# Kernel tuning notes

Hardware: AMD Instinct MI355X
Metric: run time of the kernel (lower is better)

Reference implementation:

```python
import math
import jax, jax.numpy as jnp
import numpy as np

B, N, DIM, H, DH = 2, 1024, 1024, 16, 64
SCALE = 16.0  # cosine_sim_scale
LN_EPS = 1e-5


def layer_norm(x, g, eps=LN_EPS):
    # torch: unbiased=False variance
    m = jnp.mean(x, axis=-1, keepdims=True)
    v = jnp.var(x, axis=-1, keepdims=True)
    return (x - m) * jax.lax.rsqrt(v + eps) * g


def l2norm(t):
    # F.normalize(dim=-1): x / max(||x||, 1e-12)
    n = jnp.linalg.norm(t, axis=-1, keepdims=True)
    return t / jnp.maximum(n, 1e-12)


def setup_inputs() -> dict:
    key = jax.random.key(0)
    ks = jax.random.split(key, 8)
    x = jax.random.normal(ks[0], (B, N, DIM), jnp.float32)
    attn_bias = jax.random.normal(ks[1], (B, H, N, N + 1), jnp.float32) * 0.02
    g_in = jnp.ones((DIM,), jnp.float32)
    w_q = jax.random.normal(ks[2], (H * DH, DIM), jnp.float32) * 0.02
    w_kv = jax.random.normal(ks[3], (2 * DH, DIM), jnp.float32) * 0.02
    null_kv = jax.random.normal(ks[4], (2, DH), jnp.float32)
    w_out = jax.random.normal(ks[5], (DIM, H * DH), jnp.float32) * 0.02
    g_out = jnp.ones((DIM,), jnp.float32)
    mask = jnp.ones((B, N), dtype=bool)
    return dict(x=x, attn_bias=attn_bias, g_in=g_in, w_q=w_q, w_kv=w_kv,
                null_kv=null_kv, w_out=w_out, g_out=g_out, mask=mask)


def reference(x, attn_bias, g_in, w_q, w_kv, null_kv, w_out, g_out, mask):
    b, n, _ = x.shape
    xn = layer_norm(x, g_in)
    q = xn @ w_q.T                      # [b, n, H*DH]
    kv = xn @ w_kv.T                    # [b, n, 2*DH]  (single kv head)
    k, v = kv[..., :DH], kv[..., DH:]
    q = q.reshape(b, n, H, DH).transpose(0, 2, 1, 3) * SCALE  # [b, h, n, d]
    nk = jnp.broadcast_to(null_kv[0], (b, 1, DH))
    nv = jnp.broadcast_to(null_kv[1], (b, 1, DH))
    k = jnp.concatenate([nk, k], axis=1)  # [b, n+1, d]
    v = jnp.concatenate([nv, v], axis=1)
    # cosine-sim attention: l2norm then scale by sqrt(cosine_sim_scale)
    q = l2norm(q) * math.sqrt(SCALE)
    k = l2norm(k) * math.sqrt(SCALE)
    sim = jnp.einsum('bhid,bjd->bhij', q, k) + attn_bias
    mask_p = jnp.concatenate([jnp.ones((b, 1), dtype=bool), mask], axis=1)  # null kv always visible
    max_neg = -jnp.finfo(sim.dtype).max
    sim = jnp.where(mask_p[:, None, None, :], sim, max_neg)
    attn = jax.nn.softmax(sim.astype(jnp.float32), axis=-1).astype(sim.dtype)
    out = jnp.einsum('bhij,bjd->bhid', attn, v)
    out = out.transpose(0, 2, 1, 3).reshape(b, n, H * DH)
    out = out @ w_out.T
    return layer_norm(out, g_out)
```

## Files before the change

kernel.cpp:

```cpp
#include <hip/hip_runtime.h>
#include <math.h>

#define B_   2
#define N_   1024
#define DIM_ 1024
#define H_   16
#define NK_  1025
#define NKP_ 1088

typedef __attribute__((ext_vector_type(8))) short s16x8;
typedef __attribute__((ext_vector_type(4))) float f32x4;

__device__ __forceinline__ float wave_sum(float v) {
  #pragma unroll
  for (int off = 32; off; off >>= 1) v += __shfl_xor(v, off);
  return v;
}
__device__ __forceinline__ short f2bf(float f) {
  union { float f; unsigned u; } v; v.f = f;
  unsigned r = (v.u + 0x7fffu + ((v.u >> 16) & 1u)) >> 16;
  return (short)r;
}
__device__ __forceinline__ float bf2f(short s) {
  union { unsigned u; float f; } v; v.u = ((unsigned)(unsigned short)s) << 16;
  return v.f;
}
__device__ __forceinline__ void gl_lds16(const short* g, short* lds) {
  __builtin_amdgcn_global_load_lds(
      (const __attribute__((address_space(1))) void*)g,
      (__attribute__((address_space(3))) void*)lds, 16, 0, 0);
}

__global__ __launch_bounds__(256) void cvt_all(const float* __restrict__ wq,
                                               const float* __restrict__ wkv,
                                               const float* __restrict__ wout,
                                               short* __restrict__ Wqkv,
                                               short* __restrict__ Wout) {
  int i = (blockIdx.x * 256 + threadIdx.x) * 4;
  const float* s; short* d; int k;
  if (i < 1048576)      { s = wq;   d = Wqkv;           k = i; }
  else if (i < 1179648) { s = wkv;  d = Wqkv + 1048576; k = i - 1048576; }
  else                  { s = wout; d = Wout;           k = i - 1179648; }
  float4 v = *(const float4*)&s[k];
  short4 r; r.x = f2bf(v.x); r.y = f2bf(v.y); r.z = f2bf(v.z); r.w = f2bf(v.w);
  *(short4*)&d[k] = r;
}

__global__ __launch_bounds__(256) void ln_in(const float* __restrict__ x,
                                             const float* __restrict__ g,
                                             short* __restrict__ o) {
  int row = blockIdx.x, tid = threadIdx.x;
  const float* xr = x + (size_t)row * DIM_;
  float4 v = *(const float4*)&xr[tid * 4];
  float s  = v.x + v.y + v.z + v.w;
  float sq = v.x*v.x + v.y*v.y + v.z*v.z + v.w*v.w;
  s = wave_sum(s); sq = wave_sum(sq);
  __shared__ float red[8];
  int w = tid >> 6, lane = tid & 63;
  if (lane == 0) { red[w] = s; red[4 + w] = sq; }
  __syncthreads();
  s  = red[0] + red[1] + red[2] + red[3];
  sq = red[4] + red[5] + red[6] + red[7];
  float mean = s * (1.0f / DIM_);
  float var  = sq * (1.0f / DIM_) - mean * mean;
  float inv  = rsqrtf(var + 1e-5f);
  float4 g4 = *(const float4*)&g[tid * 4];
  short4 r;
  r.x = f2bf((v.x - mean) * inv * g4.x);
  r.y = f2bf((v.y - mean) * inv * g4.y);
  r.z = f2bf((v.z - mean) * inv * g4.z);
  r.w = f2bf((v.w - mean) * inv * g4.w);
  *(short4*)&o[(size_t)row * DIM_ + tid * 4] = r;
}

__global__ __launch_bounds__(256) void ln_out(const short* __restrict__ xb,
                                              const float* __restrict__ g,
                                              float* __restrict__ o) {
  int row = blockIdx.x, tid = threadIdx.x;
  const short* xr = xb + (size_t)row * DIM_;
  short4 s4 = *(const short4*)&xr[tid * 4];
  float v0 = bf2f(s4.x), v1 = bf2f(s4.y), v2 = bf2f(s4.z), v3 = bf2f(s4.w);
  float s  = v0 + v1 + v2 + v3;
  float sq = v0*v0 + v1*v1 + v2*v2 + v3*v3;
  s = wave_sum(s); sq = wave_sum(sq);
  __shared__ float red[8];
  int w = tid >> 6, lane = tid & 63;
  if (lane == 0) { red[w] = s; red[4 + w] = sq; }
  __syncthreads();
  s  = red[0] + red[1] + red[2] + red[3];
  sq = red[4] + red[5] + red[6] + red[7];
  float mean = s * (1.0f / DIM_);
  float var  = sq * (1.0f / DIM_) - mean * mean;
  float inv  = rsqrtf(var + 1e-5f);
  float4 g4 = *(const float4*)&g[tid * 4];
  float4 r;
  r.x = (v0 - mean) * inv * g4.x;
  r.y = (v1 - mean) * inv * g4.y;
  r.z = (v2 - mean) * inv * g4.z;
  r.w = (v3 - mean) * inv * g4.w;
  *(float4*)&o[(size_t)row * DIM_ + tid * 4] = r;
}

__global__ __launch_bounds__(256) void gemm_bf(const short* __restrict__ A,
                                               const short* __restrict__ W,
                                               short* __restrict__ C,
                                               int M, int Nn, int K) {
  __shared__ short sb[2][24 * 512];
  int tid = threadIdx.x, l = tid & 63, w = tid >> 6;
  int li = l & 15, lg = l >> 4;
  int m0 = blockIdx.y * 64, n0 = blockIdx.x * 128;
  int wm = w & 1, wn = w >> 1;

  const short* src[6];
  #pragma unroll
  for (int s = 0; s < 6; ++s) {
    int c6 = w * 6 + s;
    if (c6 < 8) { int cm = c6 >> 1, ck = c6 & 1;
      src[s] = A + (size_t)(m0 + cm * 16 + li) * K + ck * 32 + lg * 8;
    } else { int cw = c6 - 8, cn = cw >> 1, ck = cw & 1;
      src[s] = W + (size_t)(n0 + cn * 16 + li) * K + ck * 32 + lg * 8;
    }
  }

  f32x4 acc[2][4];
  #pragma unroll
  for (int mi = 0; mi < 2; ++mi)
    #pragma unroll
    for (int ni = 0; ni < 4; ++ni) {
      acc[mi][ni][0] = 0.f; acc[mi][ni][1] = 0.f;
      acc[mi][ni][2] = 0.f; acc[mi][ni][3] = 0.f;
    }

  #pragma unroll
  for (int s = 0; s < 6; ++s) gl_lds16(src[s], &sb[0][(w * 6 + s) * 512]);
  __syncthreads();

  int KT = K >> 6, cur = 0;
  for (int kt = 0; kt < KT; ++kt) {
    if (kt + 1 < KT) {
      #pragma unroll
      for (int s = 0; s < 6; ++s)
        gl_lds16(src[s] + (size_t)(kt + 1) * 64, &sb[cur ^ 1][(w * 6 + s) * 512]);
    }
    const short* sc = &sb[cur][0];
    #pragma unroll
    for (int ck = 0; ck < 2; ++ck) {
      s16x8 a0 = *(const s16x8*)&sc[((wm * 2 + 0) * 2 + ck) * 512 + l * 8];
      s16x8 a1 = *(const s16x8*)&sc[((wm * 2 + 1) * 2 + ck) * 512 + l * 8];
      #pragma unroll
      for (int ni = 0; ni < 4; ++ni) {
        s16x8 bf = *(const s16x8*)&sc[(8 + (wn * 4 + ni) * 2 + ck) * 512 + l * 8];
        acc[0][ni] = __builtin_amdgcn_mfma_f32_16x16x32_bf16(a0, bf, acc[0][ni], 0, 0, 0);
        acc[1][ni] = __builtin_amdgcn_mfma_f32_16x16x32_bf16(a1, bf, acc[1][ni], 0, 0, 0);
      }
    }
    __syncthreads();
    cur ^= 1;
  }
  #pragma unroll
  for (int mi = 0; mi < 2; ++mi)
    #pragma unroll
    for (int ni = 0; ni < 4; ++ni)
      #pragma unroll
      for (int rr = 0; rr < 4; ++rr)
        C[(size_t)(m0 + wm * 32 + mi * 16 + lg * 4 + rr) * Nn
          + n0 + wn * 64 + ni * 16 + li] = f2bf(acc[mi][ni][rr]);
}

__global__ __launch_bounds__(256) void prep_all(const short* __restrict__ Cq,
                                                const float* __restrict__ nullkv,
                                                short* __restrict__ Qbh,
                                                short* __restrict__ Kf,
                                                short* __restrict__ Vf) {
  int bidx = blockIdx.x;
  int l = threadIdx.x & 63, w = threadIdx.x >> 6;
  if (bidx < 8192) {
    int gid = bidx * 4 + w;
    int m = gid >> 4, h = gid & 15;
    float v = bf2f(Cq[(size_t)m * 1152 + h * 64 + l]);
    float ss = wave_sum(v * v);
    float q = v * (4.0f / fmaxf(sqrtf(ss), 1e-12f));
    int b = m >> 10, i = m & 1023;
    Qbh[(((size_t)(b * H_ + h)) * N_ + i) * 64 + l] = f2bf(q);
  } else {
    int row = (bidx - 8192) * 4 + w;
    int b = row / NKP_, j = row % NKP_;
    float kk, vv;
    if (j == 0)       { kk = nullkv[l]; vv = nullkv[64 + l]; }
    else if (j < NK_) {
      size_t m = (size_t)b * 1024 + j - 1;
      kk = bf2f(Cq[m * 1152 + 1024 + l]);
      vv = bf2f(Cq[m * 1152 + 1088 + l]);
    } else            { kk = 0.f; vv = 0.f; }
    float n = sqrtf(wave_sum(kk * kk));
    kk = kk * (4.0f / fmaxf(n, 1e-12f));
    Kf[(((size_t)b * 68 + (j >> 4)) * 2 + (l >> 5)) * 512
       + (size_t)((((l >> 3) & 3) << 4) + (j & 15)) * 8 + (l & 7)] = f2bf(kk);
    Vf[(((size_t)b * 17 + (j >> 6)) * 8 + ((l >> 4) << 1) + ((j >> 5) & 1)) * 512
       + (size_t)((((j >> 3) & 3) << 4) + (l & 15)) * 8 + (j & 7)] = f2bf(vv);
  }
}

__global__ __launch_bounds__(256, 2) void attn_v5(const short* __restrict__ Qbh,
                                                  const short* __restrict__ Kf,
                                                  const short* __restrict__ Vf,
                                                  const float* __restrict__ bias,
                                                  short* __restrict__ O) {
  __shared__ short sb[2][16 * 512];
  __shared__ short sP[4][1024];

  int tid = threadIdx.x, l = tid & 63, w = tid >> 6;
  int li = l & 15, lg = l >> 4;
  int bid = blockIdx.x;
  int it = bid & 15, h = (bid >> 4) & 15, b = bid >> 8;
  int i0 = it * 64 + w * 16;

  const short* qbase = Qbh + (((size_t)(b * H_ + h)) * N_ + i0 + li) * 64 + lg * 8;
  s16x8 qf0 = *(const s16x8*)qbase;
  s16x8 qf1 = *(const s16x8*)(qbase + 32);

  const short* kfb = Kf + (size_t)b * 68 * 2 * 512;
  const short* vfb = Vf + (size_t)b * 17 * 8 * 512;
  const float* bptr = bias + ((size_t)(b * H_ + h) * N_ + i0 + li) * NK_;

  #pragma unroll
  for (int s = 0; s < 2; ++s) {
    gl_lds16(kfb + (2 * w + s) * 512 + l * 8, &sb[0][(2 * w + s) * 512]);
    gl_lds16(vfb + (2 * w + s) * 512 + l * 8, &sb[0][(8 + 2 * w + s) * 512]);
  }

  s16x8 kl0 = *(const s16x8*)&kfb[((size_t)64 * 2 + 0) * 512 + lg * 128];
  s16x8 kl1 = *(const s16x8*)&kfb[((size_t)64 * 2 + 1) * 512 + lg * 128];
  float se = 0.f;
  #pragma unroll
  for (int e = 0; e < 8; ++e)
    se += bf2f(qf0[e]) * bf2f(kl0[e]) + bf2f(qf1[e]) * bf2f(kl1[e]);
  se += __shfl_xor(se, 16);
  se += __shfl_xor(se, 32);
  se += bptr[1024];

  float m_ = se, l_ = 1.f;
  f32x4 o[4];
  #pragma unroll
  for (int dt = 0; dt < 4; ++dt)
    #pragma unroll
    for (int rr = 0; rr < 4; ++rr)
      o[dt][rr] = bf2f(vfb[((size_t)16 * 8 + dt * 2) * 512 + (lg * 4 + rr) * 8]);

  float4 bb[3][4];
  #pragma unroll
  for (int q4 = 0; q4 < 4; ++q4) {
    bb[0][q4] = *(const float4*)(bptr + q4 * 16 + lg * 4);
    bb[1][q4] = *(const float4*)(bptr + 64 + q4 * 16 + lg * 4);
  }
  __syncthreads();

  short* pw = &sP[w][0];

  #pragma unroll
  for (int jt = 0; jt < 16; ++jt) {
    const int cb = jt & 1;
    if (jt + 1 < 16) {
      const short* kt_ = kfb + (size_t)(jt + 1) * 8 * 512;
      const short* vt_ = vfb + (size_t)(jt + 1) * 8 * 512;
      #pragma unroll
      for (int s = 0; s < 2; ++s) {
        gl_lds16(kt_ + (2 * w + s) * 512 + l * 8, &sb[cb ^ 1][(2 * w + s) * 512]);
        gl_lds16(vt_ + (2 * w + s) * 512 + l * 8, &sb[cb ^ 1][(8 + 2 * w + s) * 512]);
      }
    }
    if (jt + 2 < 16) {
      const float* bp = bptr + (jt + 2) * 64 + lg * 4;
      #pragma unroll
      for (int q4 = 0; q4 < 4; ++q4)
        bb[(jt + 2) % 3][q4] = *(const float4*)(bp + q4 * 16);
    }

    const short* sk = &sb[cb][0];
    const short* sv = &sb[cb][8 * 512];

    f32x4 st[4];
    #pragma unroll
    for (int jt4 = 0; jt4 < 4; ++jt4) {
      s16x8 ka0 = *(const s16x8*)&sk[(jt4 * 2 + 0) * 512 + l * 8];
      s16x8 ka1 = *(const s16x8*)&sk[(jt4 * 2 + 1) * 512 + l * 8];
      f32x4 cc; cc[0] = 0.f; cc[1] = 0.f; cc[2] = 0.f; cc[3] = 0.f;
      cc = __builtin_amdgcn_mfma_f32_16x16x32_bf16(ka0, qf0, cc, 0, 0, 0);
      cc = __builtin_amdgcn_mfma_f32_16x16x32_bf16(ka1, qf1, cc, 0, 0, 0);
      st[jt4] = cc;
    }

    float vmax = -1e30f;
    #pragma unroll
    for (int jt4 = 0; jt4 < 4; ++jt4)
      #pragma unroll
      for (int rr = 0; rr < 4; ++rr) {
        st[jt4][rr] += ((const float*)&bb[jt % 3][jt4])[rr];
        vmax = fmaxf(vmax, st[jt4][rr]);
      }
    vmax = fmaxf(vmax, __shfl_xor(vmax, 16));
    vmax = fmaxf(vmax, __shfl_xor(vmax, 32));
    float mnew = fmaxf(m_, vmax);
    float cre = __expf(m_ - mnew);
    m_ = mnew;
    float psum = 0.f;
    #pragma unroll
    for (int jt4 = 0; jt4 < 4; ++jt4)
      #pragma unroll
      for (int rr = 0; rr < 4; ++rr) {
        float p = __expf(st[jt4][rr] - mnew);
        st[jt4][rr] = p;
        psum += p;
      }
    psum += __shfl_xor(psum, 16);
    psum += __shfl_xor(psum, 32);
    l_ = l_ * cre + psum;
    #pragma unroll
    for (int dt = 0; dt < 4; ++dt) {
      o[dt][0] *= cre; o[dt][1] *= cre; o[dt][2] *= cre; o[dt][3] *= cre;
    }

    #pragma unroll
    for (int jt4 = 0; jt4 < 4; ++jt4) {
      int kfw = jt4 >> 1;
      int gw  = 2 * (jt4 & 1) + (lg >> 1);
      int ew  = (lg & 1) * 4;
      int off = kfw * 512 + (gw * 16 + li) * 8 + ew;
      #pragma unroll
      for (int rr = 0; rr < 4; ++rr) pw[off + rr] = f2bf(st[jt4][rr]);
    }
    s16x8 pb0 = *(const s16x8*)&pw[l * 8];
    s16x8 pb1 = *(const s16x8*)&pw[512 + l * 8];

    #pragma unroll
    for (int dt = 0; dt < 4; ++dt) {
      s16x8 va0 = *(const s16x8*)&sv[(dt * 2 + 0) * 512 + l * 8];
      s16x8 va1 = *(const s16x8*)&sv[(dt * 2 + 1) * 512 + l * 8];
      o[dt] = __builtin_amdgcn_mfma_f32_16x16x32_bf16(va0, pb0, o[dt], 0, 0, 0);
      o[dt] = __builtin_amdgcn_mfma_f32_16x16x32_bf16(va1, pb1, o[dt], 0, 0, 0);
    }
    __syncthreads();
  }

  float inv = 1.f / l_;
  size_t obase = ((size_t)(b * N_ + i0 + li) * H_ + h) * 64;
  #pragma unroll
  for (int dt = 0; dt < 4; ++dt)
    #pragma unroll
    for (int rp = 0; rp < 2; ++rp) {
      unsigned lo = (unsigned short)f2bf(o[dt][rp * 2]     * inv);
      unsigned hi = (unsigned short)f2bf(o[dt][rp * 2 + 1] * inv);
      *(unsigned*)&O[obase + dt * 16 + lg * 4 + rp * 2] = lo | (hi << 16);
    }
}

extern "C" void kernel_launch(void* const* d_in, const int* in_sizes, int n_in,
                              void* d_out, int out_size, void* d_ws, size_t ws_size,
                              hipStream_t stream) {
  (void)in_sizes; (void)n_in; (void)out_size; (void)ws_size;
  const float* x       = (const float*)d_in[0];
  const float* bias    = (const float*)d_in[1];
  const float* g_in    = (const float*)d_in[2];
  const float* w_q     = (const float*)d_in[3];
  const float* w_kv    = (const float*)d_in[4];
  const float* null_kv = (const float*)d_in[5];
  const float* w_out   = (const float*)d_in[6];
  const float* g_out   = (const float*)d_in[7];

  char* p = (char*)d_ws;
  short* XNbf = (short*)p;
  short* Wqkv = (short*)(p + 4194304);
  short* Wout = (short*)(p + 6553600);
  short* Cbf  = (short*)(p + 8650752);
  short* Qbh  = (short*)(p + 13369344);
  short* Kf   = (short*)(p + 17563648);
  short* Vf   = (short*)(p + 17842176);
  short* AOUT = XNbf;
  short* Cout = Cbf;
  float* out  = (float*)d_out;

  cvt_all<<<2176, 256, 0, stream>>>(w_q, w_kv, w_out, Wqkv, Wout);
  ln_in<<<B_ * N_, 256, 0, stream>>>(x, g_in, XNbf);
  gemm_bf<<<dim3(9, 32), 256, 0, stream>>>(XNbf, Wqkv, Cbf, B_ * N_, 1152, DIM_);
  prep_all<<<8192 + 544, 256, 0, stream>>>(Cbf, null_kv, Qbh, Kf, Vf);
  attn_v5<<<B_ * H_ * (N_ / 64), 256, 0, stream>>>(Qbh, Kf, Vf, bias, AOUT);
  gemm_bf<<<dim3(8, 32), 256, 0, stream>>>(AOUT, Wout, Cout, B_ * N_, DIM_, DIM_);
  ln_out<<<B_ * N_, 256, 0, stream>>>(Cout, g_out, out);
}
```

Baseline: 109.3 us.

## Split attention over key halves with a merge kernel; fuse weight cast and input layernorm

The attention kernel now splits the key range into two halves per query tile. This doubles the block count from 512 to 1024 and raises launch_bounds occupancy to 4. Partial outputs are stored as bf16 along with their running max and sum, and a new merge kernel combines them. Separately, the weight conversion and input layernorm kernels are fused into one launch to save a kernel launch. The split adds an extra kernel, extra global traffic, and a bf16 rounding step on the unnormalized partials.

```diff
diff --git a/kernel.cpp b/kernel.cpp
--- a/kernel.cpp
+++ b/kernel.cpp
@@ -31,25 +31,26 @@
       (__attribute__((address_space(3))) void*)lds, 16, 0, 0);
 }
 
-__global__ __launch_bounds__(256) void cvt_all(const float* __restrict__ wq,
-                                               const float* __restrict__ wkv,
-                                               const float* __restrict__ wout,
-                                               short* __restrict__ Wqkv,
-                                               short* __restrict__ Wout) {
-  int i = (blockIdx.x * 256 + threadIdx.x) * 4;
-  const float* s; short* d; int k;
-  if (i < 1048576)      { s = wq;   d = Wqkv;           k = i; }
-  else if (i < 1179648) { s = wkv;  d = Wqkv + 1048576; k = i - 1048576; }
-  else                  { s = wout; d = Wout;           k = i - 1179648; }
-  float4 v = *(const float4*)&s[k];
-  short4 r; r.x = f2bf(v.x); r.y = f2bf(v.y); r.z = f2bf(v.z); r.w = f2bf(v.w);
-  *(short4*)&d[k] = r;
-}
-
-__global__ __launch_bounds__(256) void ln_in(const float* __restrict__ x,
+__global__ __launch_bounds__(256) void pre_k(const float* __restrict__ wq,
+                                             const float* __restrict__ wkv,
+                                             const float* __restrict__ wout,
+                                             short* __restrict__ Wqkv,
+                                             short* __restrict__ Wout,
+                                             const float* __restrict__ x,
                                              const float* __restrict__ g,
-                                             short* __restrict__ o) {
-  int row = blockIdx.x, tid = threadIdx.x;
+                                             short* __restrict__ xo) {
+  if (blockIdx.x < 2176) {
+    int i = (blockIdx.x * 256 + threadIdx.x) * 4;
+    const float* s; short* d; int k;
+    if (i < 1048576)      { s = wq;   d = Wqkv;           k = i; }
+    else if (i < 1179648) { s = wkv;  d = Wqkv + 1048576; k = i - 1048576; }
+    else                  { s = wout; d = Wout;           k = i - 1179648; }
+    float4 v = *(const float4*)&s[k];
+    short4 r; r.x = f2bf(v.x); r.y = f2bf(v.y); r.z = f2bf(v.z); r.w = f2bf(v.w);
+    *(short4*)&d[k] = r;
+    return;
+  }
+  int row = blockIdx.x - 2176, tid = threadIdx.x;
   const float* xr = x + (size_t)row * DIM_;
   float4 v = *(const float4*)&xr[tid * 4];
   float s  = v.x + v.y + v.z + v.w;
@@ -70,7 +71,7 @@
   r.y = f2bf((v.y - mean) * inv * g4.y);
   r.z = f2bf((v.z - mean) * inv * g4.z);
   r.w = f2bf((v.w - mean) * inv * g4.w);
-  *(short4*)&o[(size_t)row * DIM_ + tid * 4] = r;
+  *(short4*)&xo[(size_t)row * DIM_ + tid * 4] = r;
 }
 
 __global__ __launch_bounds__(256) void ln_out(const short* __restrict__ xb,
@@ -201,19 +202,22 @@
   }
 }
 
-__global__ __launch_bounds__(256, 2) void attn_v5(const short* __restrict__ Qbh,
+__global__ __launch_bounds__(256, 4) void attn_v6(const short* __restrict__ Qbh,
                                                   const short* __restrict__ Kf,
                                                   const short* __restrict__ Vf,
                                                   const float* __restrict__ bias,
-                                                  short* __restrict__ O) {
+                                                  short* __restrict__ Opart,
+                                                  float* __restrict__ Mp,
+                                                  float* __restrict__ Lp) {
   __shared__ short sb[2][16 * 512];
   __shared__ short sP[4][1024];
 
   int tid = threadIdx.x, l = tid & 63, w = tid >> 6;
   int li = l & 15, lg = l >> 4;
   int bid = blockIdx.x;
-  int it = bid & 15, h = (bid >> 4) & 15, b = bid >> 8;
+  int half = bid & 1, it = (bid >> 1) & 15, h = (bid >> 5) & 15, b = bid >> 9;
   int i0 = it * 64 + w * 16;
+  const int t0 = half * 8;
 
   const short* qbase = Qbh + (((size_t)(b * H_ + h)) * N_ + i0 + li) * 64 + lg * 8;
   s16x8 qf0 = *(const s16x8*)qbase;
@@ -223,44 +227,55 @@
   const short* vfb = Vf + (size_t)b * 17 * 8 * 512;
   const float* bptr = bias + ((size_t)(b * H_ + h) * N_ + i0 + li) * NK_;
 
-  #pragma unroll
-  for (int s = 0; s < 2; ++s) {
-    gl_lds16(kfb + (2 * w + s) * 512 + l * 8, &sb[0][(2 * w + s) * 512]);
-    gl_lds16(vfb + (2 * w + s) * 512 + l * 8, &sb[0][(8 + 2 * w + s) * 512]);
-  }
-
-  s16x8 kl0 = *(const s16x8*)&kfb[((size_t)64 * 2 + 0) * 512 + lg * 128];
-  s16x8 kl1 = *(const s16x8*)&kfb[((size_t)64 * 2 + 1) * 512 + lg * 128];
-  float se = 0.f;
-  #pragma unroll
-  for (int e = 0; e < 8; ++e)
-    se += bf2f(qf0[e]) * bf2f(kl0[e]) + bf2f(qf1[e]) * bf2f(kl1[e]);
-  se += __shfl_xor(se, 16);
-  se += __shfl_xor(se, 32);
-  se += bptr[1024];
-
-  float m_ = se, l_ = 1.f;
+  {
+    const short* kt_ = kfb + (size_t)t0 * 8 * 512;
+    const short* vt_ = vfb + (size_t)t0 * 8 * 512;
+    #pragma unroll
+    for (int s = 0; s < 2; ++s) {
+      gl_lds16(kt_ + (2 * w + s) * 512 + l * 8, &sb[0][(2 * w + s) * 512]);
+      gl_lds16(vt_ + (2 * w + s) * 512 + l * 8, &sb[0][(8 + 2 * w + s) * 512]);
+    }
+  }
+
+  float m_, l_;
   f32x4 o[4];
-  #pragma unroll
-  for (int dt = 0; dt < 4; ++dt)
-    #pragma unroll
-    for (int rr = 0; rr < 4; ++rr)
-      o[dt][rr] = bf2f(vfb[((size_t)16 * 8 + dt * 2) * 512 + (lg * 4 + rr) * 8]);
-
-  float4 bb[3][4];
-  #pragma unroll
-  for (int q4 = 0; q4 < 4; ++q4) {
-    bb[0][q4] = *(const float4*)(bptr + q4 * 16 + lg * 4);
-    bb[1][q4] = *(const float4*)(bptr + 64 + q4 * 16 + lg * 4);
-  }
+  if (half == 0) {
+    s16x8 kl0 = *(const s16x8*)&kfb[((size_t)64 * 2 + 0) * 512 + lg * 128];
+    s16x8 kl1 = *(const s16x8*)&kfb[((size_t)64 * 2 + 1) * 512 + lg * 128];
+    float se = 0.f;
+    #pragma unroll
+    for (int e = 0; e < 8; ++e)
+      se += bf2f(qf0[e]) * bf2f(kl0[e]) + bf2f(qf1[e]) * bf2f(kl1[e]);
+    se += __shfl_xor(se, 16);
+    se += __shfl_xor(se, 32);
+    se += bptr[1024];
+    m_ = se; l_ = 1.f;
+    #pragma unroll
+    for (int dt = 0; dt < 4; ++dt)
+      #pragma unroll
+      for (int rr = 0; rr < 4; ++rr)
+        o[dt][rr] = bf2f(vfb[((size_t)16 * 8 + dt * 2) * 512 + (lg * 4 + rr) * 8]);
+  } else {
+    m_ = -1e30f; l_ = 0.f;
+    #pragma unroll
+    for (int dt = 0; dt < 4; ++dt) {
+      o[dt][0] = 0.f; o[dt][1] = 0.f; o[dt][2] = 0.f; o[dt][3] = 0.f;
+    }
+  }
+
+  float4 bb[2][4];
+  #pragma unroll
+  for (int q4 = 0; q4 < 4; ++q4)
+    bb[0][q4] = *(const float4*)(bptr + t0 * 64 + q4 * 16 + lg * 4);
   __syncthreads();
 
   short* pw = &sP[w][0];
 
   #pragma unroll
-  for (int jt = 0; jt < 16; ++jt) {
-    const int cb = jt & 1;
-    if (jt + 1 < 16) {
+  for (int t = 0; t < 8; ++t) {
+    const int cb = t & 1;
+    const int jt = t0 + t;
+    if (t + 1 < 8) {
       const short* kt_ = kfb + (size_t)(jt + 1) * 8 * 512;
       const short* vt_ = vfb + (size_t)(jt + 1) * 8 * 512;
       #pragma unroll
@@ -268,12 +283,10 @@
         gl_lds16(kt_ + (2 * w + s) * 512 + l * 8, &sb[cb ^ 1][(2 * w + s) * 512]);
         gl_lds16(vt_ + (2 * w + s) * 512 + l * 8, &sb[cb ^ 1][(8 + 2 * w + s) * 512]);
       }
-    }
-    if (jt + 2 < 16) {
-      const float* bp = bptr + (jt + 2) * 64 + lg * 4;
+      const float* bp = bptr + (jt + 1) * 64 + lg * 4;
       #pragma unroll
       for (int q4 = 0; q4 < 4; ++q4)
-        bb[(jt + 2) % 3][q4] = *(const float4*)(bp + q4 * 16);
+        bb[(t + 1) & 1][q4] = *(const float4*)(bp + q4 * 16);
     }
 
     const short* sk = &sb[cb][0];
@@ -295,7 +308,7 @@
     for (int jt4 = 0; jt4 < 4; ++jt4)
       #pragma unroll
       for (int rr = 0; rr < 4; ++rr) {
-        st[jt4][rr] += ((const float*)&bb[jt % 3][jt4])[rr];
+        st[jt4][rr] += ((const float*)&bb[t & 1][jt4])[rr];
         vmax = fmaxf(vmax, st[jt4][rr]);
       }
     vmax = fmaxf(vmax, __shfl_xor(vmax, 16));
@@ -342,14 +355,53 @@
     __syncthreads();
   }
 
-  float inv = 1.f / l_;
+  size_t slot = (size_t)bid * 256 + tid;
+  Mp[slot] = m_;
+  Lp[slot] = l_;
+  short* op = Opart + slot * 16;
+  #pragma unroll
+  for (int dt = 0; dt < 4; ++dt)
+    #pragma unroll
+    for (int rp = 0; rp < 2; ++rp) {
+      unsigned lo = (unsigned short)f2bf(o[dt][rp * 2]);
+      unsigned hi = (unsigned short)f2bf(o[dt][rp * 2 + 1]);
+      *(unsigned*)&op[dt * 4 + rp * 2] = lo | (hi << 16);
+    }
+}
+
+__global__ __launch_bounds__(256) void merge_k(const short* __restrict__ Opart,
+                                               const float* __restrict__ Mp,
+                                               const float* __restrict__ Lp,
+                                               short* __restrict__ O) {
+  int grp = blockIdx.x;
+  int s = threadIdx.x;
+  int it = grp & 15, h = (grp >> 4) & 15, b = grp >> 8;
+  size_t s0 = ((size_t)grp * 2 + 0) * 256 + s;
+  size_t s1 = ((size_t)grp * 2 + 1) * 256 + s;
+  float m0 = Mp[s0], m1 = Mp[s1];
+  float l0 = Lp[s0], l1 = Lp[s1];
+  float ms = fmaxf(m0, m1);
+  float f0 = __expf(m0 - ms), f1 = __expf(m1 - ms);
+  float inv = 1.0f / (l0 * f0 + l1 * f1);
+  f0 *= inv; f1 *= inv;
+  s16x8 o0a = *(const s16x8*)&Opart[s0 * 16];
+  s16x8 o0b = *(const s16x8*)&Opart[s0 * 16 + 8];
+  s16x8 o1a = *(const s16x8*)&Opart[s1 * 16];
+  s16x8 o1b = *(const s16x8*)&Opart[s1 * 16 + 8];
+  int w = s >> 6, l = s & 63, li = l & 15, lg = l >> 4;
+  int i0 = it * 64 + w * 16;
   size_t obase = ((size_t)(b * N_ + i0 + li) * H_ + h) * 64;
   #pragma unroll
   for (int dt = 0; dt < 4; ++dt)
     #pragma unroll
     for (int rp = 0; rp < 2; ++rp) {
-      unsigned lo = (unsigned short)f2bf(o[dt][rp * 2]     * inv);
-      unsigned hi = (unsigned short)f2bf(o[dt][rp * 2 + 1] * inv);
+      int k = dt * 4 + rp * 2;
+      float v0 = (k < 8 ? bf2f(o0a[k & 7]) : bf2f(o0b[k & 7])) * f0
+               + (k < 8 ? bf2f(o1a[k & 7]) : bf2f(o1b[k & 7])) * f1;
+      float v1 = (k + 1 < 8 ? bf2f(o0a[(k + 1) & 7]) : bf2f(o0b[(k + 1) & 7])) * f0
+               + (k + 1 < 8 ? bf2f(o1a[(k + 1) & 7]) : bf2f(o1b[(k + 1) & 7])) * f1;
+      unsigned lo = (unsigned short)f2bf(v0);
+      unsigned hi = (unsigned short)f2bf(v1);
       *(unsigned*)&O[obase + dt * 16 + lg * 4 + rp * 2] = lo | (hi << 16);
     }
 }
@@ -375,15 +427,18 @@
   short* Qbh  = (short*)(p + 13369344);
   short* Kf   = (short*)(p + 17563648);
   short* Vf   = (short*)(p + 17842176);
+  short* Opart= (short*)(p + 18120704);
+  float* Mp   = (float*)(p + 26509312);
+  float* Lp   = (float*)(p + 27557888);
   short* AOUT = XNbf;
   short* Cout = Cbf;
   float* out  = (float*)d_out;
 
-  cvt_all<<<2176, 256, 0, stream>>>(w_q, w_kv, w_out, Wqkv, Wout);
-  ln_in<<<B_ * N_, 256, 0, stream>>>(x, g_in, XNbf);
+  pre_k<<<2176 + 2048, 256, 0, stream>>>(w_q, w_kv, w_out, Wqkv, Wout, x, g_in, XNbf);
   gemm_bf<<<dim3(9, 32), 256, 0, stream>>>(XNbf, Wqkv, Cbf, B_ * N_, 1152, DIM_);
   prep_all<<<8192 + 544, 256, 0, stream>>>(Cbf, null_kv, Qbh, Kf, Vf);
-  attn_v5<<<B_ * H_ * (N_ / 64), 256, 0, stream>>>(Qbh, Kf, Vf, bias, AOUT);
+  attn_v6<<<B_ * H_ * (N_ / 64) * 2, 256, 0, stream>>>(Qbh, Kf, Vf, bias, Opart, Mp, Lp);
+  merge_k<<<B_ * H_ * (N_ / 64), 256, 0, stream>>>(Opart, Mp, Lp, AOUT);
   gemm_bf<<<dim3(8, 32), 256, 0, stream>>>(AOUT, Wout, Cout, B_ * N_, DIM_, DIM_);
   ln_out<<<B_ * N_, 256, 0, stream>>>(Cout, g_out, out);
 }
```

After: 121.9 us. +11.6%, slower.
